# Optimization experiments

Measured on AMD Instinct MI355X. Metric: run time of the kernel, lower is better.

The kernel has to match this reference:

```python
import jax, jax.numpy as jnp
import numpy as np

ETA = 0.5
R_CUTOFF = 6.0
ZETA = 0.6
LAMDA = 0.8
RS = 1.0
SPECIAL_ATOM = 8  # atom index routed to elem2 net


def _af(x):
    return 1.0 / (1.0 + x * x)


def _mlp(g, w1, b1, w2, b2, w3, b3):
    h = _af(g @ w1.T + b1)
    h = _af(h @ w2.T + b2)
    return h @ w3.T + b3  # [N,1]


def setup_inputs() -> dict:
    key = jax.random.key(0)
    ks = jax.random.split(key, 13)
    N = 384
    x = jax.random.normal(ks[0], (N, 3), dtype=jnp.float32) * 2.0
    def lin(kw, kb, fout, fin):
        w = jax.random.normal(kw, (fout, fin), dtype=jnp.float32) * (1.0 / np.sqrt(fin))
        b = jax.random.normal(kb, (fout,), dtype=jnp.float32) * 0.1
        return w, b
    w1a, b1a = lin(ks[1], ks[2], 40, 2)
    w2a, b2a = lin(ks[3], ks[4], 40, 40)
    w3a, b3a = lin(ks[5], ks[6], 1, 40)
    w1b, b1b = lin(ks[7], ks[8], 40, 2)
    w2b, b2b = lin(ks[9], ks[10], 40, 40)
    w3b, b3b = lin(ks[11], ks[12], 1, 40)
    return {"x": x,
            "w1a": w1a, "b1a": b1a, "w2a": w2a, "b2a": b2a, "w3a": w3a, "b3a": b3a,
            "w1b": w1b, "b1b": b1b, "w2b": w2b, "b2b": b2b, "w3b": w3b, "b3b": b3b}


def _descriptors(x):
    N = x.shape[0]
    eye = jnp.eye(N, dtype=bool)
    diff = x[:, None, :] - x[None, :, :]           # [N,N,3]
    D2 = jnp.sum(diff * diff, axis=-1)             # [N,N]
    D = jnp.sqrt(jnp.where(eye, 1.0, D2))
    D = jnp.where(eye, 0.0, D)
    # cutoff function (hard 0 beyond R_cutoff), zeroed on diagonal
    fc = jnp.where((D <= R_CUTOFF) & (~eye), 0.5 * (jnp.cos(np.pi * D / R_CUTOFF) + 1.0), 0.0)
    # radial symmetry function per atom i
    rad = jnp.sum(jnp.exp(-ETA * (D - RS) ** 2) * fc, axis=1)  # [N]
    # angular: sum over triplets j<k, j!=i, k!=i
    A = jnp.exp(-ETA * D2) * fc                    # [N,N], zero on diagonal
    Gm = x @ x.T                                   # Gram matrix
    gd = jnp.diag(Gm)
    # dot(Rij, Rki) with Rij = x_i - x_j, Rki = x_k - x_i
    dot = Gm[:, None, :] - gd[:, None, None] - Gm[None, :, :] + Gm[:, :, None]  # [N,N,N] (i,j,k)
    denom = D[:, :, None] * D[:, None, :]          # |Rij| * |Rki|
    cos_theta = dot / jnp.where(denom > 0, denom, 1.0)
    term1 = jnp.maximum(1.0 + LAMDA * cos_theta, 1e-6) ** ZETA
    # A[i,j] * A[j,k] * A[k,i]; diag-zero A kills i==j and i==k terms
    term2 = A[:, :, None] * A[None, :, :] * A[:, None, :]
    tri = jnp.triu(jnp.ones((N, N), dtype=jnp.float32), k=1)[None, :, :]  # j < k
    ang = (2.0 ** (1.0 - ZETA)) * jnp.sum(term1 * term2 * tri, axis=(1, 2))  # [N]
    return jnp.stack([ang, rad], axis=-1)          # [N,2], order matches Gi=[ang, rad]


def reference(x, w1a, b1a, w2a, b2a, w3a, b3a, w1b, b1b, w2b, b2b, w3b, b3b):
    G = _descriptors(x)
    q1 = _mlp(G, w1a, b1a, w2a, b2a, w3a, b3a)[:, 0]
    q2 = _mlp(G, w1b, b1b, w2b, b2b, w3b, b3b)[:, 0]
    idx = jnp.arange(x.shape[0])
    return jnp.where(idx == SPECIAL_ATOM, q2, q1)  # [N]
```

## Files before the change

### kernel.cpp

```cpp
#include <hip/hip_runtime.h>
#include <math.h>

#define N 384
#define EPSA 1e-4f

#if __has_builtin(__builtin_amdgcn_logf) && __has_builtin(__builtin_amdgcn_exp2f)
#define LOG2F(x) __builtin_amdgcn_logf(x)
#define EXP2F(x) __builtin_amdgcn_exp2f(x)
#else
#define LOG2F(x) __log2f(x)
#define EXP2F(x) __expf(0.69314718056f * (x))
#endif

__device__ __forceinline__ float wave_reduce(float v) {
#pragma unroll
    for (int o = 32; o > 0; o >>= 1) v += __shfl_down(v, o, 64);
    return v;
}

__global__ __launch_bounds__(128) void pair_kernel(
    const float* __restrict__ x, float* __restrict__ A,
    float4* __restrict__ nbr4, int* __restrict__ nbrJ, int* __restrict__ cnt,
    float* __restrict__ rad, float* __restrict__ ang) {
    const int i = blockIdx.x;
    const int t = threadIdx.x;
    const int lane = t & 63, w = t >> 6;
    const float xi0 = x[3 * i + 0], xi1 = x[3 * i + 1], xi2 = x[3 * i + 2];

    float racc = 0.0f;
    float4 val[3];
    int keep[3];
#pragma unroll
    for (int r = 0; r < 3; ++r) {
        const int j = t + 128 * r;
        float dx = xi0 - x[3 * j + 0];
        float dy = xi1 - x[3 * j + 1];
        float dz = xi2 - x[3 * j + 2];
        float d2 = dx * dx + dy * dy + dz * dz;
        float a = 0.0f, rr = 0.0f, inv = 0.0f;
        if (j != i) {
            float d = sqrtf(d2);
            if (d <= 6.0f) {
                float fc = 0.5f * (__cosf(0.52359877559829887f * d) + 1.0f);
                a = __expf(-0.5f * d2) * fc;
                float dm = d - 1.0f;
                rr = __expf(-0.5f * dm * dm) * fc;
            }
            inv = rsqrtf(d2);
        }
        A[i * N + j] = a;
        racc += rr;
        val[r] = make_float4(dx * inv, dy * inv, dz * inv, a);
        keep[r] = (a > EPSA) ? 1 : 0;
    }

    __shared__ int bcnt[6], bbase[6];
    int pfx[3];
#pragma unroll
    for (int r = 0; r < 3; ++r) {
        unsigned long long m = __ballot(keep[r]);
        pfx[r] = __popcll(m & ((1ull << lane) - 1ull));
        if (lane == 0) bcnt[w + 2 * r] = __popcll(m);
    }
    __syncthreads();
    if (t == 0) {
        int s = 0;
#pragma unroll
        for (int c = 0; c < 6; ++c) { bbase[c] = s; s += bcnt[c]; }
        cnt[i] = s;
        ang[i] = 0.0f;
    }
    __syncthreads();
#pragma unroll
    for (int r = 0; r < 3; ++r) {
        if (keep[r]) {
            const int slot = bbase[w + 2 * r] + pfx[r];
            nbr4[i * N + slot] = val[r];
            nbrJ[i * N + slot] = t + 128 * r;
        }
    }

    __shared__ float red[2];
    float v = wave_reduce(racc);
    if (lane == 0) red[w] = v;
    __syncthreads();
    if (t == 0) rad[i] = red[0] + red[1];
}

__global__ __launch_bounds__(256) void ang_kernel(
    const float* __restrict__ A, const float4* __restrict__ nbr4,
    const int* __restrict__ nbrJ, const int* __restrict__ cnt,
    float* __restrict__ ang) {
    const int i = blockIdx.x;
    const int jc = blockIdx.y;
    const int t = threadIdx.x;
    const int n = cnt[i];
    if (n == 0) return;

    const int qn = (n + 3) >> 2;
    const int js = jc * qn;
    const int je = min(js + qn, n);
    if (js >= je) return;
    const int m = je - js;

    __shared__ __align__(16) float4 sh4[96];
    __shared__ int shJN[96];
    for (int s = t; s < m; s += 256) {
        sh4[s] = nbr4[i * N + js + s];
        shJN[s] = nbrJ[i * N + js + s] * N;
    }
    __syncthreads();

    float acc = 0.0f;
    for (int ks0 = 0; ks0 < n; ks0 += 256) {
        const int ks = ks0 + t;
        const int valid = ks < n;
        float4 K = valid ? nbr4[i * N + ks] : make_float4(0.f, 0.f, 0.f, 0.f);
        const int kcol = valid ? nbrJ[i * N + ks] : 0;
        const float kx = -0.8f * K.x, ky = -0.8f * K.y, kz = -0.8f * K.z;
        const float kA = K.w;
        const float* Acol = A + kcol;

        float cacc = 0.0f;
        int ro = __builtin_amdgcn_readfirstlane(shJN[0]);
        float a = Acol[ro];
#pragma unroll 2
        for (int s = 0; s < m; ++s) {
            int rn = __builtin_amdgcn_readfirstlane(shJN[min(s + 1, m - 1)]);
            float an = Acol[rn];
            float4 J = sh4[s];
            float b = fmaf(J.x, kx, fmaf(J.y, ky, fmaf(J.z, kz, 1.0f)));
            float p = EXP2F(0.6f * LOG2F(b));
            cacc = fmaf(J.w * a, p, cacc);
            a = an;
        }
        acc = fmaf(kA, cacc, acc);
    }

    __shared__ float red[4];
    float v = wave_reduce(acc);
    if ((t & 63) == 0) red[t >> 6] = v;
    __syncthreads();
    if (t == 0) atomicAdd(&ang[i], red[0] + red[1] + red[2] + red[3]);
}

#define WSTRIDE 1804
__global__ __launch_bounds__(64) void mlp_kernel(
    const float* __restrict__ ang, const float* __restrict__ rad,
    float* __restrict__ out,
    const float* w1a, const float* b1a, const float* w2a, const float* b2a,
    const float* w3a, const float* b3a, const float* w1b, const float* b1b,
    const float* w2b, const float* b2b, const float* w3b, const float* b3b) {
    __shared__ __align__(16) float W[2 * WSTRIDE];
    const int t = threadIdx.x;
    {
        const float* srcs[12] = {w1a, b1a, w2a, b2a, w3a, b3a,
                                 w1b, b1b, w2b, b2b, w3b, b3b};
        const int ns[6] = {80, 40, 1600, 40, 40, 1};
        const int offs[6] = {0, 80, 120, 1720, 1760, 1800};
        for (int s = 0; s < 12; ++s) {
            const int base = (s / 6) * WSTRIDE + offs[s % 6];
            const int n4 = ns[s % 6] >> 2;
            const float4* src4 = (const float4*)srcs[s];
            float4* dst4 = (float4*)(W + base);
            for (int q = t; q < n4; q += 64) dst4[q] = src4[q];
        }
        if (t == 0) {
            W[1800] = b3a[0];
            W[WSTRIDE + 1800] = b3b[0];
        }
    }
    __syncthreads();

    const int atom = blockIdx.x * 16 + (t >> 2);
    const int net = (t >> 1) & 1;
    const int half = t & 1;
    const float* P = W + net * WSTRIDE;

    const float g0 = 0.6597539553864471f * ang[atom];
    const float g1 = rad[atom];

    float h1[40];
#pragma unroll
    for (int u = 0; u < 40; ++u) {
        float z = fmaf(P[2 * u], g0, fmaf(P[2 * u + 1], g1, P[80 + u]));
        h1[u] = 1.0f / fmaf(z, z, 1.0f);
    }

    float acc = half ? 0.0f : P[1800];
    const int v0 = half * 20;
    for (int v2 = v0; v2 < v0 + 20; ++v2) {
        const float4* row = (const float4*)(P + 120 + v2 * 40);
        float z0 = P[1720 + v2], z1 = 0.0f, z2 = 0.0f, z3 = 0.0f;
#pragma unroll
        for (int q = 0; q < 10; ++q) {
            float4 r = row[q];
            z0 = fmaf(r.x, h1[4 * q + 0], z0);
            z1 = fmaf(r.y, h1[4 * q + 1], z1);
            z2 = fmaf(r.z, h1[4 * q + 2], z2);
            z3 = fmaf(r.w, h1[4 * q + 3], z3);
        }
        float z = (z0 + z1) + (z2 + z3);
        float h = 1.0f / fmaf(z, z, 1.0f);
        acc = fmaf(P[1760 + v2], h, acc);
    }
    acc += __shfl_down(acc, 1, 64);

    if (half == 0 && net == ((atom == 8) ? 1 : 0)) out[atom] = acc;
}

extern "C" void kernel_launch(void* const* d_in, const int* in_sizes, int n_in,
                              void* d_out, int out_size, void* d_ws, size_t ws_size,
                              hipStream_t stream) {
    const float* x = (const float*)d_in[0];
    const float* w1a = (const float*)d_in[1];
    const float* b1a = (const float*)d_in[2];
    const float* w2a = (const float*)d_in[3];
    const float* b2a = (const float*)d_in[4];
    const float* w3a = (const float*)d_in[5];
    const float* b3a = (const float*)d_in[6];
    const float* w1b = (const float*)d_in[7];
    const float* b1b = (const float*)d_in[8];
    const float* w2b = (const float*)d_in[9];
    const float* b2b = (const float*)d_in[10];
    const float* w3b = (const float*)d_in[11];
    const float* b3b = (const float*)d_in[12];
    float* out = (float*)d_out;

    float* ws = (float*)d_ws;
    float* A = ws;
    float4* nbr4 = (float4*)(ws + 147456);
    int* nbrJ = (int*)(ws + 147456 + 4 * 147456);
    float* rad = ws + 147456 * 6;
    float* ang = rad + 384;
    int* cnt = (int*)(ang + 384);

    hipLaunchKernelGGL(pair_kernel, dim3(N), dim3(128), 0, stream,
                       x, A, nbr4, nbrJ, cnt, rad, ang);
    hipLaunchKernelGGL(ang_kernel, dim3(N, 4), dim3(256), 0, stream,
                       A, nbr4, nbrJ, cnt, ang);
    hipLaunchKernelGGL(mlp_kernel, dim3(24), dim3(64), 0, stream,
                       ang, rad, out,
                       w1a, b1a, w2a, b2a, w3a, b3a,
                       w1b, b1b, w2b, b2b, w3b, b3b);
}
```

Before: 112.8 us.

## Pad neighbor lists to multiples of eight and batch A gathers in ang kernel

The pair kernel now pads each atom's neighbor list to a multiple of 8 with zero-weight dummy entries pointing at the atom itself. The angular kernel drops the shared-memory staging of its j-chunk. Each block instead walks 8-wide j-groups strided across the four y-blocks, issuing eight A-column gathers up front before the pow computations. This removes a sync and the per-iteration readfirstlane dependency chain, aiming for more memory-level parallelism. In exchange it reads j data straight from global memory via uniform loads and does some padded work.

```diff
diff --git a/kernel.cpp b/kernel.cpp
--- a/kernel.cpp
+++ b/kernel.cpp
@@ -54,7 +54,7 @@
         keep[r] = (a > EPSA) ? 1 : 0;
     }
 
-    __shared__ int bcnt[6], bbase[6];
+    __shared__ int bcnt[6], bbase[6], realn;
     int pfx[3];
 #pragma unroll
     for (int r = 0; r < 3; ++r) {
@@ -67,7 +67,8 @@
         int s = 0;
 #pragma unroll
         for (int c = 0; c < 6; ++c) { bbase[c] = s; s += bcnt[c]; }
-        cnt[i] = s;
+        realn = s;
+        cnt[i] = (s + 7) & ~7;
         ang[i] = 0.0f;
     }
     __syncthreads();
@@ -78,6 +79,12 @@
             nbr4[i * N + slot] = val[r];
             nbrJ[i * N + slot] = t + 128 * r;
         }
+    }
+    const int rn = realn;
+    const int np = (rn + 7) & ~7;
+    if (t < np - rn) {
+        nbr4[i * N + rn + t] = make_float4(0.f, 0.f, 0.f, 0.f);
+        nbrJ[i * N + rn + t] = i;
     }
 
     __shared__ float red[2];
@@ -96,43 +103,33 @@
     const int t = threadIdx.x;
     const int n = cnt[i];
     if (n == 0) return;
-
-    const int qn = (n + 3) >> 2;
-    const int js = jc * qn;
-    const int je = min(js + qn, n);
-    if (js >= je) return;
-    const int m = je - js;
-
-    __shared__ __align__(16) float4 sh4[96];
-    __shared__ int shJN[96];
-    for (int s = t; s < m; s += 256) {
-        sh4[s] = nbr4[i * N + js + s];
-        shJN[s] = nbrJ[i * N + js + s] * N;
-    }
-    __syncthreads();
+    const int iN = i * N;
+    const int nb = n >> 3;
 
     float acc = 0.0f;
     for (int ks0 = 0; ks0 < n; ks0 += 256) {
         const int ks = ks0 + t;
-        const int valid = ks < n;
-        float4 K = valid ? nbr4[i * N + ks] : make_float4(0.f, 0.f, 0.f, 0.f);
-        const int kcol = valid ? nbrJ[i * N + ks] : 0;
+        const bool valid = ks < n;
+        float4 K = valid ? nbr4[iN + ks] : make_float4(0.f, 0.f, 0.f, 0.f);
+        const int kcol = valid ? nbrJ[iN + ks] : 0;
         const float kx = -0.8f * K.x, ky = -0.8f * K.y, kz = -0.8f * K.z;
         const float kA = K.w;
         const float* Acol = A + kcol;
 
         float cacc = 0.0f;
-        int ro = __builtin_amdgcn_readfirstlane(shJN[0]);
-        float a = Acol[ro];
-#pragma unroll 2
-        for (int s = 0; s < m; ++s) {
-            int rn = __builtin_amdgcn_readfirstlane(shJN[min(s + 1, m - 1)]);
-            float an = Acol[rn];
-            float4 J = sh4[s];
-            float b = fmaf(J.x, kx, fmaf(J.y, ky, fmaf(J.z, kz, 1.0f)));
-            float p = EXP2F(0.6f * LOG2F(b));
-            cacc = fmaf(J.w * a, p, cacc);
-            a = an;
+        for (int b = jc; b < nb; b += 4) {
+            const int s0 = b << 3;
+            float a8[8];
+#pragma unroll
+            for (int q = 0; q < 8; ++q)
+                a8[q] = Acol[nbrJ[iN + s0 + q] * N];
+#pragma unroll
+            for (int q = 0; q < 8; ++q) {
+                float4 J = nbr4[iN + s0 + q];
+                float bb = fmaf(J.x, kx, fmaf(J.y, ky, fmaf(J.z, kz, 1.0f)));
+                float p = EXP2F(0.6f * LOG2F(bb));
+                cacc = fmaf(J.w * a8[q], p, cacc);
+            }
         }
         acc = fmaf(kA, cacc, acc);
     }
```

Measured after the change: 111.0 us. Within noise of the previous version (-1.5%).
